# Kernel tuning notes

Measured on AMD Instinct MI355X. Metric: run time of the kernel, lower is better.

## Reference

```python
import jax, jax.numpy as jnp
import numpy as np

N_CELL, N_DRUG = 8192, 4096
E_CELL, E_DRUG = 262144, 131072
D_OUT = 128


def setup_inputs() -> dict:
    key = jax.random.key(0)
    ks = jax.random.split(key, 8)
    cell_feat = jax.random.normal(ks[0], (N_CELL, N_CELL), dtype=jnp.float32)
    drug_feat = jax.random.normal(ks[1], (N_DRUG, N_DRUG), dtype=jnp.float32)
    cell_edge = jax.random.randint(ks[2], (2, E_CELL), 0, N_CELL, dtype=jnp.int64)
    drug_edge = jax.random.randint(ks[3], (2, E_DRUG), 0, N_DRUG, dtype=jnp.int64)
    W_cell = jax.random.normal(ks[4], (N_CELL, D_OUT), dtype=jnp.float32) * 0.02
    W_drug = jax.random.normal(ks[5], (N_DRUG, D_OUT), dtype=jnp.float32) * 0.02
    b_cell = jnp.zeros((D_OUT,), dtype=jnp.float32)
    b_drug = jnp.zeros((D_OUT,), dtype=jnp.float32)
    return {"cell_feat": cell_feat, "cell_edge": cell_edge, "W_cell": W_cell,
            "b_cell": b_cell, "drug_feat": drug_feat, "drug_edge": drug_edge,
            "W_drug": W_drug, "b_drug": b_drug}


def _gcn_conv(x, edge, W, b):
    """PyG GCNConv with edge_weight = x[row, col] (as in GEncoder.forward),
    add_self_loops=True, symmetric normalization."""
    N = x.shape[0]
    row, col = edge[0], edge[1]
    ew = x[row, col]                                  # [E] gathered edge weights
    loop = jnp.arange(N)
    row = jnp.concatenate([row, loop])                # [E+N] self-loops appended
    col = jnp.concatenate([col, loop])
    ew = jnp.concatenate([ew, jnp.ones((N,), x.dtype)])
    deg = jax.ops.segment_sum(ew, col, num_segments=N)
    dinv = jnp.where(deg > 0, jax.lax.rsqrt(jnp.maximum(deg, 1e-30)), 0.0)
    norm = dinv[row] * ew * dinv[col]                 # [E+N]
    h = x @ W                                         # [N, D_OUT]
    msg = norm[:, None] * h[row]                      # gather + scale
    out = jax.ops.segment_sum(msg, col, num_segments=N) + b
    return jax.nn.relu(out)


def reference(cell_feat, cell_edge, W_cell, b_cell, drug_feat, drug_edge, W_drug, b_drug):
    cell_gcn = _gcn_conv(cell_feat, cell_edge, W_cell, b_cell)
    drug_gcn = _gcn_conv(drug_feat, drug_edge, W_drug, b_drug)
    return (cell_gcn, drug_gcn)
```

## Files before the change

kernel.cpp:

```cpp
#include <hip/hip_runtime.h>
#include <stdint.h>

#define N_CELL 8192
#define N_DRUG 4096
#define E_CELL 262144
#define E_DRUG 131072
#define DOUT   128

typedef float f32x4 __attribute__((ext_vector_type(4)));
typedef short s16x8 __attribute__((ext_vector_type(8)));

#define OFF_DEG_C   0u
#define OFF_DEG_D   8192u
#define OFF_CNT_C   12288u
#define OFF_CNT_D   20480u
#define OFF_CUR_C   24576u
#define OFF_CUR_D   32768u
#define OFF_START_C 36864u
#define OFF_START_D 45312u
#define OFF_EW_C    49664u
#define OFF_EW_D    311808u
#define OFF_SROW_C  442880u
#define OFF_SROW_D  705024u
#define OFF_SCOEF_C 836096u
#define OFF_SCOEF_D 1098240u
#define OFF_H_C     1229312u
#define OFF_H_D     2277888u
#define OFF_END     2802176u
#define WT_C_BYTE   (OFF_END * 4u)
#define WT_D_BYTE   (WT_C_BYTE + 128u * 8192u * 2u)
#define PART_C_BYTE 14354432u
#define PART_D_BYTE 31131648u
#define PART_END    35325952u

__device__ __forceinline__ unsigned short f2bf(float f) {
    union { float f; uint32_t u; } v; v.f = f;
    uint32_t u = v.u + 0x7fffu + ((v.u >> 16) & 1u);
    return (unsigned short)(u >> 16);
}

__device__ __forceinline__ s16x8 pack8(float4 x, float4 y) {
    union { float4 f; uint32_t u[4]; } a, b;
    a.f = x; b.f = y;
    union { uint32_t u[4]; s16x8 v; } r;
    r.u[0] = __builtin_amdgcn_perm(a.u[1] + 0x8000u, a.u[0] + 0x8000u, 0x07060302u);
    r.u[1] = __builtin_amdgcn_perm(a.u[3] + 0x8000u, a.u[2] + 0x8000u, 0x07060302u);
    r.u[2] = __builtin_amdgcn_perm(b.u[1] + 0x8000u, b.u[0] + 0x8000u, 0x07060302u);
    r.u[3] = __builtin_amdgcn_perm(b.u[3] + 0x8000u, b.u[2] + 0x8000u, 0x07060302u);
    return r.v;
}

__global__ __launch_bounds__(256) void k_prep(const float* __restrict__ Wc, const float* __restrict__ Wd,
                                              unsigned short* __restrict__ wtc, unsigned short* __restrict__ wtd,
                                              float* __restrict__ ws) {
    int bid = blockIdx.x, t = threadIdx.x;
    if (bid < 144) {
        int i = bid * 256 + t;
        ws[i] = (i < 12288) ? 1.0f : 0.0f;
        return;
    }
    if (bid < 1680) {
        size_t i = (size_t)(bid - 144) * 256 + t;
        ((float4*)(ws + OFF_H_C))[i] = make_float4(0.f, 0.f, 0.f, 0.f);
        return;
    }
    int tile = bid - 1680;
    const float* W; unsigned short* wt; int K;
    if (tile < 1024) { W = Wc; wt = wtc; K = N_CELL; }
    else             { W = Wd; wt = wtd; K = N_DRUG; tile -= 1024; }
    int tk = tile >> 2, tc = tile & 3;
    __shared__ float tl[32][33];
    int c = t & 31, r8 = t >> 5;
#pragma unroll
    for (int p = 0; p < 4; ++p) {
        int row = r8 + p * 8;
        tl[row][c] = W[(size_t)(tk * 32 + row) * DOUT + tc * 32 + c];
    }
    __syncthreads();
#pragma unroll
    for (int p = 0; p < 4; ++p) {
        int c2 = r8 + p * 8;
        wt[(size_t)(tc * 32 + c2) * K + tk * 32 + c] = f2bf(tl[c][c2]);
    }
}

__global__ __launch_bounds__(256) void k_edge(const float* __restrict__ xc, const int* __restrict__ ec,
                                              const float* __restrict__ xd, const int* __restrict__ ed,
                                              float* __restrict__ ws) {
    int i = blockIdx.x * 256 + threadIdx.x;
    const float* x; const int* edges; float* ew; float* deg; int* cnt; int N, E, idx;
    if (i < E_CELL) {
        idx = i; x = xc; edges = ec; N = N_CELL; E = E_CELL;
        ew = ws + OFF_EW_C; deg = ws + OFF_DEG_C; cnt = (int*)(ws + OFF_CNT_C);
    } else {
        idx = i - E_CELL; if (idx >= E_DRUG) return;
        x = xd; edges = ed; N = N_DRUG; E = E_DRUG;
        ew = ws + OFF_EW_D; deg = ws + OFF_DEG_D; cnt = (int*)(ws + OFF_CNT_D);
    }
    int r = edges[idx], c = edges[E + idx];
    float w = x[(size_t)r * N + c];
    ew[idx] = w;
    unsafeAtomicAdd(&deg[c], w);
    atomicAdd(&cnt[c], 1);
}

__global__ __launch_bounds__(256) void k_scan2(float* ws) {
    int bid = blockIdx.x, t = threadIdx.x;
    if (bid < 48) {
        int i = bid * 256 + t;
        float d = ws[i];
        ws[i] = d > 0.f ? rsqrtf(fmaxf(d, 1e-30f)) : 0.f;
        return;
    }
    const int* cnt; int* start; int N, chunk;
    if (bid == 48) { cnt = (const int*)(ws + OFF_CNT_C); start = (int*)(ws + OFF_START_C); N = N_CELL; chunk = 32; }
    else           { cnt = (const int*)(ws + OFF_CNT_D); start = (int*)(ws + OFF_START_D); N = N_DRUG; chunk = 16; }
    __shared__ int sums[256];
    int base = t * chunk;
    int s = 0;
    for (int j = 0; j < chunk; ++j) s += cnt[base + j];
    sums[t] = s; __syncthreads();
    for (int off = 1; off < 256; off <<= 1) {
        int v = (t >= off) ? sums[t - off] : 0;
        __syncthreads();
        sums[t] += v;
        __syncthreads();
    }
    int run = sums[t] - s;
    for (int j = 0; j < chunk; ++j) { start[base + j] = run; run += cnt[base + j]; }
    if (t == 255) start[N] = run;
}

__global__ __launch_bounds__(256) void k_fill(const int* __restrict__ ec, const int* __restrict__ ed,
                                              float* __restrict__ ws) {
    int i = blockIdx.x * 256 + threadIdx.x;
    const int* edges; const float* ew; const float* dinv; const int* start;
    int* cur; int* srow; float* scoef; int E, idx;
    if (i < E_CELL) {
        idx = i; edges = ec; E = E_CELL;
        ew = ws + OFF_EW_C; dinv = ws + OFF_DEG_C; start = (const int*)(ws + OFF_START_C);
        cur = (int*)(ws + OFF_CUR_C); srow = (int*)(ws + OFF_SROW_C); scoef = ws + OFF_SCOEF_C;
    } else {
        idx = i - E_CELL; if (idx >= E_DRUG) return;
        edges = ed; E = E_DRUG;
        ew = ws + OFF_EW_D; dinv = ws + OFF_DEG_D; start = (const int*)(ws + OFF_START_D);
        cur = (int*)(ws + OFF_CUR_D); srow = (int*)(ws + OFF_SROW_D); scoef = ws + OFF_SCOEF_D;
    }
    int r = edges[idx], c = edges[E + idx];
    float coef = dinv[r] * ew[idx] * dinv[c];
    int slot = start[c] + atomicAdd(&cur[c], 1);
    srow[slot] = r;
    scoef[slot] = coef;
}

__global__ __launch_bounds__(256, 6) void k_gemm(const float* __restrict__ xc, const float* __restrict__ xd,
                                                 const unsigned short* __restrict__ wtc,
                                                 const unsigned short* __restrict__ wtd,
                                                 float* __restrict__ ws,
                                                 float* __restrict__ partC, float* __restrict__ partD,
                                                 int usePart) {
    int bid = blockIdx.x, t = threadIdx.x;
    const float* x; const unsigned short* wt; float* hp; float* part; int K, mt, ch; size_t pstride;
    if (bid < 1024) {
        x = xc; wt = wtc; hp = ws + OFF_H_C; part = partC; K = N_CELL;
        mt = bid >> 2; ch = bid & 3; pstride = (size_t)N_CELL * DOUT;
    } else {
        int b = bid - 1024; x = xd; wt = wtd; hp = ws + OFF_H_D; part = partD; K = N_DRUG;
        mt = b >> 1; ch = b & 1; pstride = (size_t)N_DRUG * DOUT;
    }
    int k0 = ch * 2048;

    __shared__ alignas(16) unsigned short As[2][32][72];
    int lane = t & 63, wv = t >> 6;
    int l15 = lane & 15, l4 = lane >> 4;

    f32x4 acc[2][2] = {};

    int srow = t >> 3, sseg = t & 7;
    const float* abase = x + (size_t)(mt * 32 + srow) * K + k0 + sseg * 8;
    const unsigned short* bb = wt + (size_t)(wv * 32 + l15) * K + k0 + l4 * 8;
    const unsigned short* bb1 = bb + (size_t)16 * K;

    float4 X0, X1;

#define LOADA(KT) { const float4* _p = (const float4*)(abase + (size_t)(KT) * 64); \
                    X0 = _p[0]; X1 = _p[1]; }
#define WRITEA(BUF) { *(s16x8*)&As[BUF][srow][sseg * 8] = pack8(X0, X1); }

    LOADA(0);
    WRITEA(0);
    LOADA(1);
    __syncthreads();

#pragma unroll 1
    for (int kt = 0; kt < 32; ++kt) {
        s16x8 bq00 = *(const s16x8*)(bb  + (size_t)kt * 64);
        s16x8 bq01 = *(const s16x8*)(bb  + (size_t)kt * 64 + 32);
        s16x8 bq10 = *(const s16x8*)(bb1 + (size_t)kt * 64);
        s16x8 bq11 = *(const s16x8*)(bb1 + (size_t)kt * 64 + 32);
        if (kt < 31) {
            WRITEA((kt + 1) & 1);
            if (kt < 30) LOADA(kt + 2);
        }
        int bf = kt & 1;
        {
            s16x8 a0 = *(const s16x8*)&As[bf][l15][l4 * 8];
            s16x8 a1 = *(const s16x8*)&As[bf][16 + l15][l4 * 8];
            acc[0][0] = __builtin_amdgcn_mfma_f32_16x16x32_bf16(a0, bq00, acc[0][0], 0, 0, 0);
            acc[0][1] = __builtin_amdgcn_mfma_f32_16x16x32_bf16(a0, bq10, acc[0][1], 0, 0, 0);
            acc[1][0] = __builtin_amdgcn_mfma_f32_16x16x32_bf16(a1, bq00, acc[1][0], 0, 0, 0);
            acc[1][1] = __builtin_amdgcn_mfma_f32_16x16x32_bf16(a1, bq10, acc[1][1], 0, 0, 0);
        }
        {
            s16x8 a0 = *(const s16x8*)&As[bf][l15][32 + l4 * 8];
            s16x8 a1 = *(const s16x8*)&As[bf][16 + l15][32 + l4 * 8];
            acc[0][0] = __builtin_amdgcn_mfma_f32_16x16x32_bf16(a0, bq01, acc[0][0], 0, 0, 0);
            acc[0][1] = __builtin_amdgcn_mfma_f32_16x16x32_bf16(a0, bq11, acc[0][1], 0, 0, 0);
            acc[1][0] = __builtin_amdgcn_mfma_f32_16x16x32_bf16(a1, bq01, acc[1][0], 0, 0, 0);
            acc[1][1] = __builtin_amdgcn_mfma_f32_16x16x32_bf16(a1, bq11, acc[1][1], 0, 0, 0);
        }
        __syncthreads();
    }
#undef LOADA
#undef WRITEA
    if (usePart) {
        float* dst = part + (size_t)ch * pstride;
#pragma unroll
        for (int m = 0; m < 2; ++m)
#pragma unroll
            for (int n = 0; n < 2; ++n) {
                int col = wv * 32 + n * 16 + l15;
                int row = mt * 32 + m * 16 + l4 * 4;
#pragma unroll
                for (int j = 0; j < 4; ++j)
                    dst[(size_t)(row + j) * DOUT + col] = acc[m][n][j];
            }
    } else {
#pragma unroll
        for (int m = 0; m < 2; ++m)
#pragma unroll
            for (int n = 0; n < 2; ++n) {
                int col = wv * 32 + n * 16 + l15;
                int row = mt * 32 + m * 16 + l4 * 4;
#pragma unroll
                for (int j = 0; j < 4; ++j)
                    unsafeAtomicAdd(&hp[(size_t)(row + j) * DOUT + col], acc[m][n][j]);
            }
    }
}

__global__ __launch_bounds__(256) void k_reduce(const float* __restrict__ partC,
                                                const float* __restrict__ partD,
                                                float* __restrict__ ws) {
    int bid = blockIdx.x, t = threadIdx.x;
    if (bid < 1024) {
        size_t i = (size_t)bid * 256 + t;
        const f32x4* p = (const f32x4*)partC;
        f32x4 s = p[i] + p[i + 262144] + p[i + 2 * 262144] + p[i + 3 * 262144];
        ((f32x4*)(ws + OFF_H_C))[i] = s;
    } else {
        size_t i = (size_t)(bid - 1024) * 256 + t;
        const f32x4* p = (const f32x4*)partD;
        f32x4 s = p[i] + p[i + 131072];
        ((f32x4*)(ws + OFF_H_D))[i] = s;
    }
}

__global__ __launch_bounds__(256) void k_gather(const float* __restrict__ ws,
                                                const float* __restrict__ bc, const float* __restrict__ bd,
                                                float* __restrict__ out) {
    int wv = threadIdx.x >> 6, lane = threadIdx.x & 63;
    int g = blockIdx.x * 4 + wv;
    const float* h; const int* srow; const float* scoef; const int* start; const float* dinv;
    const float* bvec; float* outp; int node;
    if (g < N_CELL) {
        node = g; h = ws + OFF_H_C; srow = (const int*)(ws + OFF_SROW_C); scoef = ws + OFF_SCOEF_C;
        start = (const int*)(ws + OFF_START_C); dinv = ws + OFF_DEG_C; bvec = bc; outp = out;
    } else {
        node = g - N_CELL; if (node >= N_DRUG) return;
        h = ws + OFF_H_D; srow = (const int*)(ws + OFF_SROW_D); scoef = ws + OFF_SCOEF_D;
        start = (const int*)(ws + OFF_START_D); dinv = ws + OFF_DEG_D; bvec = bd;
        outp = out + (size_t)N_CELL * DOUT;
    }
    float di = dinv[node], sc = di * di;
    float2 v = ((const float2*)(h + (size_t)node * DOUT))[lane];
    float ax = sc * v.x, ay = sc * v.y;
    int s0 = start[node], s1 = start[node + 1];
    int e = s0;
    for (; e + 3 < s1; e += 4) {
        int r0 = srow[e];     float c0 = scoef[e];
        int r1 = srow[e + 1]; float c1 = scoef[e + 1];
        int r2 = srow[e + 2]; float c2 = scoef[e + 2];
        int r3 = srow[e + 3]; float c3 = scoef[e + 3];
        float2 u0 = ((const float2*)(h + (size_t)r0 * DOUT))[lane];
        float2 u1 = ((const float2*)(h + (size_t)r1 * DOUT))[lane];
        float2 u2 = ((const float2*)(h + (size_t)r2 * DOUT))[lane];
        float2 u3 = ((const float2*)(h + (size_t)r3 * DOUT))[lane];
        ax += c0 * u0.x + c1 * u1.x + c2 * u2.x + c3 * u3.x;
        ay += c0 * u0.y + c1 * u1.y + c2 * u2.y + c3 * u3.y;
    }
    for (; e < s1; ++e) {
        int r = srow[e]; float cf = scoef[e];
        float2 u = ((const float2*)(h + (size_t)r * DOUT))[lane];
        ax += cf * u.x; ay += cf * u.y;
    }
    float2 bb = ((const float2*)bvec)[lane];
    ax = fmaxf(ax + bb.x, 0.f);
    ay = fmaxf(ay + bb.y, 0.f);
    float2 o; o.x = ax; o.y = ay;
    ((float2*)outp)[(size_t)node * 64 + lane] = o;
}

extern "C" void kernel_launch(void* const* d_in, const int* in_sizes, int n_in,
                              void* d_out, int out_size, void* d_ws, size_t ws_size,
                              hipStream_t stream) {
    const float* cell_feat = (const float*)d_in[0];
    const int*   cell_edge = (const int*)d_in[1];
    const float* W_cell    = (const float*)d_in[2];
    const float* b_cell    = (const float*)d_in[3];
    const float* drug_feat = (const float*)d_in[4];
    const int*   drug_edge = (const int*)d_in[5];
    const float* W_drug    = (const float*)d_in[6];
    const float* b_drug    = (const float*)d_in[7];
    float* out = (float*)d_out;
    float* ws  = (float*)d_ws;
    unsigned short* wtc = (unsigned short*)((char*)d_ws + WT_C_BYTE);
    unsigned short* wtd = (unsigned short*)((char*)d_ws + WT_D_BYTE);
    float* partC = (float*)((char*)d_ws + PART_C_BYTE);
    float* partD = (float*)((char*)d_ws + PART_D_BYTE);
    int usePart = (ws_size >= (size_t)PART_END) ? 1 : 0;

    k_prep<<<3216, 256, 0, stream>>>(W_cell, W_drug, wtc, wtd, ws);
    k_edge<<<(E_CELL + E_DRUG) / 256, 256, 0, stream>>>(cell_feat, cell_edge, drug_feat, drug_edge, ws);
    k_scan2<<<50, 256, 0, stream>>>(ws);
    k_fill<<<1536, 256, 0, stream>>>(cell_edge, drug_edge, ws);
    k_gemm<<<1280, 256, 0, stream>>>(cell_feat, drug_feat, wtc, wtd, ws, partC, partD, usePart);
    if (usePart) k_reduce<<<1536, 256, 0, stream>>>(partC, partD, ws);
    k_gather<<<3072, 256, 0, stream>>>(ws, b_cell, b_drug, out);
}
```

Measured before the change: 240.6 us.

## Widen GEMM K-tile to 128 and double-buffer B fragments in registers

```diff
diff --git a/kernel.cpp b/kernel.cpp
--- a/kernel.cpp
+++ b/kernel.cpp
@@ -153,7 +153,7 @@
     scoef[slot] = coef;
 }
 
-__global__ __launch_bounds__(256, 6) void k_gemm(const float* __restrict__ xc, const float* __restrict__ xd,
+__global__ __launch_bounds__(256, 3) void k_gemm(const float* __restrict__ xc, const float* __restrict__ xd,
                                                  const unsigned short* __restrict__ wtc,
                                                  const unsigned short* __restrict__ wtd,
                                                  float* __restrict__ ws,
@@ -170,81 +170,110 @@
     }
     int k0 = ch * 2048;
 
-    __shared__ alignas(16) unsigned short As[2][32][72];
+    __shared__ alignas(16) unsigned short As[2][32][136];
     int lane = t & 63, wv = t >> 6;
     int l15 = lane & 15, l4 = lane >> 4;
 
-    f32x4 acc[2][2] = {};
+    f32x4 acc00 = {}, acc01 = {}, acc10 = {}, acc11 = {};
 
     int srow = t >> 3, sseg = t & 7;
-    const float* abase = x + (size_t)(mt * 32 + srow) * K + k0 + sseg * 8;
-    const unsigned short* bb = wt + (size_t)(wv * 32 + l15) * K + k0 + l4 * 8;
+    const float* abase = x + (size_t)(mt * 32 + srow) * K + k0 + sseg * 16;
+    const unsigned short* bb  = wt + (size_t)(wv * 32 + l15) * K + k0 + l4 * 8;
     const unsigned short* bb1 = bb + (size_t)16 * K;
 
-    float4 X0, X1;
-
-#define LOADA(KT) { const float4* _p = (const float4*)(abase + (size_t)(KT) * 64); \
-                    X0 = _p[0]; X1 = _p[1]; }
-#define WRITEA(BUF) { *(s16x8*)&As[BUF][srow][sseg * 8] = pack8(X0, X1); }
+    float4 X0, X1, X2, X3;
+    s16x8 BA0, BA1, BA2, BA3, BA4, BA5, BA6, BA7;
+    s16x8 BB0, BB1, BB2, BB3, BB4, BB5, BB6, BB7;
+
+#define LOADA(IT) { const float4* _p = (const float4*)(abase + (size_t)(IT) * 128); \
+                    X0 = _p[0]; X1 = _p[1]; X2 = _p[2]; X3 = _p[3]; }
+#define WRITEA(BUF) { *(s16x8*)&As[BUF][srow][sseg * 16]     = pack8(X0, X1); \
+                      *(s16x8*)&As[BUF][srow][sseg * 16 + 8] = pack8(X2, X3); }
+#define BLOADM(P0,P1,P2,P3,P4,P5,P6,P7, IT) { \
+    P0 = *(const s16x8*)(bb  + (size_t)(IT) * 128); \
+    P1 = *(const s16x8*)(bb  + (size_t)(IT) * 128 + 32); \
+    P2 = *(const s16x8*)(bb  + (size_t)(IT) * 128 + 64); \
+    P3 = *(const s16x8*)(bb  + (size_t)(IT) * 128 + 96); \
+    P4 = *(const s16x8*)(bb1 + (size_t)(IT) * 128); \
+    P5 = *(const s16x8*)(bb1 + (size_t)(IT) * 128 + 32); \
+    P6 = *(const s16x8*)(bb1 + (size_t)(IT) * 128 + 64); \
+    P7 = *(const s16x8*)(bb1 + (size_t)(IT) * 128 + 96); }
+#define COMPUTEM(BUF, B0,B1,B2,B3,B4,B5,B6,B7) { \
+    { s16x8 a0 = *(const s16x8*)&As[BUF][l15][l4 * 8]; \
+      s16x8 a1 = *(const s16x8*)&As[BUF][16 + l15][l4 * 8]; \
+      acc00 = __builtin_amdgcn_mfma_f32_16x16x32_bf16(a0, B0, acc00, 0, 0, 0); \
+      acc01 = __builtin_amdgcn_mfma_f32_16x16x32_bf16(a0, B4, acc01, 0, 0, 0); \
+      acc10 = __builtin_amdgcn_mfma_f32_16x16x32_bf16(a1, B0, acc10, 0, 0, 0); \
+      acc11 = __builtin_amdgcn_mfma_f32_16x16x32_bf16(a1, B4, acc11, 0, 0, 0); } \
+    { s16x8 a0 = *(const s16x8*)&As[BUF][l15][32 + l4 * 8]; \
+      s16x8 a1 = *(const s16x8*)&As[BUF][16 + l15][32 + l4 * 8]; \
+      acc00 = __builtin_amdgcn_mfma_f32_16x16x32_bf16(a0, B1, acc00, 0, 0, 0); \
+      acc01 = __builtin_amdgcn_mfma_f32_16x16x32_bf16(a0, B5, acc01, 0, 0, 0); \
+      acc10 = __builtin_amdgcn_mfma_f32_16x16x32_bf16(a1, B1, acc10, 0, 0, 0); \
+      acc11 = __builtin_amdgcn_mfma_f32_16x16x32_bf16(a1, B5, acc11, 0, 0, 0); } \
+    { s16x8 a0 = *(const s16x8*)&As[BUF][l15][64 + l4 * 8]; \
+      s16x8 a1 = *(const s16x8*)&As[BUF][16 + l15][64 + l4 * 8]; \
+      acc00 = __builtin_amdgcn_mfma_f32_16x16x32_bf16(a0, B2, acc00, 0, 0, 0); \
+      acc01 = __builtin_amdgcn_mfma_f32_16x16x32_bf16(a0, B6, acc01, 0, 0, 0); \
+      acc10 = __builtin_amdgcn_mfma_f32_16x16x32_bf16(a1, B2, acc10, 0, 0, 0); \
+      acc11 = __builtin_amdgcn_mfma_f32_16x16x32_bf16(a1, B6, acc11, 0, 0, 0); } \
+    { s16x8 a0 = *(const s16x8*)&As[BUF][l15][96 + l4 * 8]; \
+      s16x8 a1 = *(const s16x8*)&As[BUF][16 + l15][96 + l4 * 8]; \
+      acc00 = __builtin_amdgcn_mfma_f32_16x16x32_bf16(a0, B3, acc00, 0, 0, 0); \
+      acc01 = __builtin_amdgcn_mfma_f32_16x16x32_bf16(a0, B7, acc01, 0, 0, 0); \
+      acc10 = __builtin_amdgcn_mfma_f32_16x16x32_bf16(a1, B3, acc10, 0, 0, 0); \
+      acc11 = __builtin_amdgcn_mfma_f32_16x16x32_bf16(a1, B7, acc11, 0, 0, 0); } }
 
     LOADA(0);
     WRITEA(0);
     LOADA(1);
+    BLOADM(BA0,BA1,BA2,BA3,BA4,BA5,BA6,BA7, 0);
     __syncthreads();
 
 #pragma unroll 1
-    for (int kt = 0; kt < 32; ++kt) {
-        s16x8 bq00 = *(const s16x8*)(bb  + (size_t)kt * 64);
-        s16x8 bq01 = *(const s16x8*)(bb  + (size_t)kt * 64 + 32);
-        s16x8 bq10 = *(const s16x8*)(bb1 + (size_t)kt * 64);
-        s16x8 bq11 = *(const s16x8*)(bb1 + (size_t)kt * 64 + 32);
-        if (kt < 31) {
-            WRITEA((kt + 1) & 1);
-            if (kt < 30) LOADA(kt + 2);
+    for (int it2 = 0; it2 < 8; ++it2) {
+        int itE = it2 * 2, itO = itE + 1;
+        BLOADM(BB0,BB1,BB2,BB3,BB4,BB5,BB6,BB7, itO);
+        WRITEA(itO & 1);
+        if (itE < 14) LOADA(itE + 2);
+        COMPUTEM(itE & 1, BA0,BA1,BA2,BA3,BA4,BA5,BA6,BA7);
+        __syncthreads();
+        if (itO < 15) {
+            BLOADM(BA0,BA1,BA2,BA3,BA4,BA5,BA6,BA7, itO + 1);
+            WRITEA((itO + 1) & 1);
+            if (itO < 14) LOADA(itO + 2);
         }
-        int bf = kt & 1;
-        {
-            s16x8 a0 = *(const s16x8*)&As[bf][l15][l4 * 8];
-            s16x8 a1 = *(const s16x8*)&As[bf][16 + l15][l4 * 8];
-            acc[0][0] = __builtin_amdgcn_mfma_f32_16x16x32_bf16(a0, bq00, acc[0][0], 0, 0, 0);
-            acc[0][1] = __builtin_amdgcn_mfma_f32_16x16x32_bf16(a0, bq10, acc[0][1], 0, 0, 0);
-            acc[1][0] = __builtin_amdgcn_mfma_f32_16x16x32_bf16(a1, bq00, acc[1][0], 0, 0, 0);
-            acc[1][1] = __builtin_amdgcn_mfma_f32_16x16x32_bf16(a1, bq10, acc[1][1], 0, 0, 0);
-        }
-        {
-            s16x8 a0 = *(const s16x8*)&As[bf][l15][32 + l4 * 8];
-            s16x8 a1 = *(const s16x8*)&As[bf][16 + l15][32 + l4 * 8];
-            acc[0][0] = __builtin_amdgcn_mfma_f32_16x16x32_bf16(a0, bq01, acc[0][0], 0, 0, 0);
-            acc[0][1] = __builtin_amdgcn_mfma_f32_16x16x32_bf16(a0, bq11, acc[0][1], 0, 0, 0);
-            acc[1][0] = __builtin_amdgcn_mfma_f32_16x16x32_bf16(a1, bq01, acc[1][0], 0, 0, 0);
-            acc[1][1] = __builtin_amdgcn_mfma_f32_16x16x32_bf16(a1, bq11, acc[1][1], 0, 0, 0);
-        }
+        COMPUTEM(itO & 1, BB0,BB1,BB2,BB3,BB4,BB5,BB6,BB7);
         __syncthreads();
     }
 #undef LOADA
 #undef WRITEA
+#undef BLOADM
+#undef COMPUTEM
     if (usePart) {
         float* dst = part + (size_t)ch * pstride;
 #pragma unroll
         for (int m = 0; m < 2; ++m)
 #pragma unroll
             for (int n = 0; n < 2; ++n) {
+                f32x4 a = (m == 0) ? (n == 0 ? acc00 : acc01) : (n == 0 ? acc10 : acc11);
                 int col = wv * 32 + n * 16 + l15;
                 int row = mt * 32 + m * 16 + l4 * 4;
 #pragma unroll
                 for (int j = 0; j < 4; ++j)
-                    dst[(size_t)(row + j) * DOUT + col] = acc[m][n][j];
+                    dst[(size_t)(row + j) * DOUT + col] = a[j];
             }
     } else {
 #pragma unroll
         for (int m = 0; m < 2; ++m)
 #pragma unroll
             for (int n = 0; n < 2; ++n) {
+                f32x4 a = (m == 0) ? (n == 0 ? acc00 : acc01) : (n == 0 ? acc10 : acc11);
                 int col = wv * 32 + n * 16 + l15;
                 int row = mt * 32 + m * 16 + l4 * 4;
 #pragma unroll
                 for (int j = 0; j < 4; ++j)
-                    unsafeAtomicAdd(&hp[(size_t)(row + j) * DOUT + col], acc[m][n][j]);
+                    unsafeAtomicAdd(&hp[(size_t)(row + j) * DOUT + col], a[j]);
             }
     }
 }
```

Measured after the change: 228.2 us. 5.1% less time.

## Retile GEMM to 128-row blocks with LDS-staged weights and deeper split-K

Applied to the files above, without the earlier changes.

```diff
diff --git a/kernel.cpp b/kernel.cpp
--- a/kernel.cpp
+++ b/kernel.cpp
@@ -30,8 +30,8 @@
 #define WT_C_BYTE   (OFF_END * 4u)
 #define WT_D_BYTE   (WT_C_BYTE + 128u * 8192u * 2u)
 #define PART_C_BYTE 14354432u
-#define PART_D_BYTE 31131648u
-#define PART_END    35325952u
+#define PART_D_BYTE 47908864u
+#define PART_END    56297472u
 
 __device__ __forceinline__ unsigned short f2bf(float f) {
     union { float f; uint32_t u; } v; v.f = f;
@@ -153,98 +153,86 @@
     scoef[slot] = coef;
 }
 
-__global__ __launch_bounds__(256, 6) void k_gemm(const float* __restrict__ xc, const float* __restrict__ xd,
-                                                 const unsigned short* __restrict__ wtc,
-                                                 const unsigned short* __restrict__ wtd,
-                                                 float* __restrict__ ws,
-                                                 float* __restrict__ partC, float* __restrict__ partD,
-                                                 int usePart) {
+__global__ __launch_bounds__(256, 2) void k_gemm2(const float* __restrict__ xc, const float* __restrict__ xd,
+                                                  const unsigned short* __restrict__ wtc,
+                                                  const unsigned short* __restrict__ wtd,
+                                                  float* __restrict__ ws,
+                                                  float* __restrict__ partC, float* __restrict__ partD,
+                                                  int usePart) {
     int bid = blockIdx.x, t = threadIdx.x;
     const float* x; const unsigned short* wt; float* hp; float* part; int K, mt, ch; size_t pstride;
-    if (bid < 1024) {
+    if (bid < 512) {
         x = xc; wt = wtc; hp = ws + OFF_H_C; part = partC; K = N_CELL;
-        mt = bid >> 2; ch = bid & 3; pstride = (size_t)N_CELL * DOUT;
-    } else {
-        int b = bid - 1024; x = xd; wt = wtd; hp = ws + OFF_H_D; part = partD; K = N_DRUG;
-        mt = b >> 1; ch = b & 1; pstride = (size_t)N_DRUG * DOUT;
-    }
-    int k0 = ch * 2048;
-
-    __shared__ alignas(16) unsigned short As[2][32][72];
+        mt = bid >> 3; ch = bid & 7; pstride = (size_t)N_CELL * DOUT;
+    } else {
+        int b = bid - 512; x = xd; wt = wtd; hp = ws + OFF_H_D; part = partD; K = N_DRUG;
+        mt = b >> 2; ch = b & 3; pstride = (size_t)N_DRUG * DOUT;
+    }
+    int k0 = ch << 10;
+    int rowbase = mt * 128;
+
+    __shared__ unsigned short Bs[128 * 264];
     int lane = t & 63, wv = t >> 6;
     int l15 = lane & 15, l4 = lane >> 4;
 
-    f32x4 acc[2][2] = {};
-
-    int srow = t >> 3, sseg = t & 7;
-    const float* abase = x + (size_t)(mt * 32 + srow) * K + k0 + sseg * 8;
-    const unsigned short* bb = wt + (size_t)(wv * 32 + l15) * K + k0 + l4 * 8;
-    const unsigned short* bb1 = bb + (size_t)16 * K;
-
-    float4 X0, X1;
-
-#define LOADA(KT) { const float4* _p = (const float4*)(abase + (size_t)(KT) * 64); \
-                    X0 = _p[0]; X1 = _p[1]; }
-#define WRITEA(BUF) { *(s16x8*)&As[BUF][srow][sseg * 8] = pack8(X0, X1); }
-
-    LOADA(0);
-    WRITEA(0);
-    LOADA(1);
-    __syncthreads();
+    f32x4 acc[2][8] = {};
+    s16x8 af[2][8];
+
+    int bcol = t >> 1, bhalf = t & 1;
+    const unsigned short* bsrc = wt + (size_t)bcol * K + k0 + bhalf * 128;
+    unsigned bdst = (unsigned)bcol * 264u + (unsigned)bhalf * 128u;
+    int arow0 = rowbase + wv * 32 + l15;
+    const float* ap0 = x + (size_t)arow0 * K + k0 + l4 * 8;
+    const float* ap1 = ap0 + (size_t)16 * K;
 
 #pragma unroll 1
-    for (int kt = 0; kt < 32; ++kt) {
-        s16x8 bq00 = *(const s16x8*)(bb  + (size_t)kt * 64);
-        s16x8 bq01 = *(const s16x8*)(bb  + (size_t)kt * 64 + 32);
-        s16x8 bq10 = *(const s16x8*)(bb1 + (size_t)kt * 64);
-        s16x8 bq11 = *(const s16x8*)(bb1 + (size_t)kt * 64 + 32);
-        if (kt < 31) {
-            WRITEA((kt + 1) & 1);
-            if (kt < 30) LOADA(kt + 2);
+    for (int kc = 0; kc < 4; ++kc) {
+        __syncthreads();
+#pragma unroll
+        for (int j = 0; j < 16; ++j) {
+            s16x8 v = *(const s16x8*)(bsrc + kc * 256 + j * 8);
+            *(s16x8*)&Bs[bdst + (unsigned)j * 8u] = v;
         }
-        int bf = kt & 1;
-        {
-            s16x8 a0 = *(const s16x8*)&As[bf][l15][l4 * 8];
-            s16x8 a1 = *(const s16x8*)&As[bf][16 + l15][l4 * 8];
-            acc[0][0] = __builtin_amdgcn_mfma_f32_16x16x32_bf16(a0, bq00, acc[0][0], 0, 0, 0);
-            acc[0][1] = __builtin_amdgcn_mfma_f32_16x16x32_bf16(a0, bq10, acc[0][1], 0, 0, 0);
-            acc[1][0] = __builtin_amdgcn_mfma_f32_16x16x32_bf16(a1, bq00, acc[1][0], 0, 0, 0);
-            acc[1][1] = __builtin_amdgcn_mfma_f32_16x16x32_bf16(a1, bq10, acc[1][1], 0, 0, 0);
-        }
-        {
-            s16x8 a0 = *(const s16x8*)&As[bf][l15][32 + l4 * 8];
-            s16x8 a1 = *(const s16x8*)&As[bf][16 + l15][32 + l4 * 8];
-            acc[0][0] = __builtin_amdgcn_mfma_f32_16x16x32_bf16(a0, bq01, acc[0][0], 0, 0, 0);
-            acc[0][1] = __builtin_amdgcn_mfma_f32_16x16x32_bf16(a0, bq11, acc[0][1], 0, 0, 0);
-            acc[1][0] = __builtin_amdgcn_mfma_f32_16x16x32_bf16(a1, bq01, acc[1][0], 0, 0, 0);
-            acc[1][1] = __builtin_amdgcn_mfma_f32_16x16x32_bf16(a1, bq11, acc[1][1], 0, 0, 0);
+#pragma unroll
+        for (int js = 0; js < 8; ++js) {
+            const float4* p0 = (const float4*)(ap0 + kc * 256 + js * 32);
+            const float4* p1 = (const float4*)(ap1 + kc * 256 + js * 32);
+            af[0][js] = pack8(p0[0], p0[1]);
+            af[1][js] = pack8(p1[0], p1[1]);
         }
         __syncthreads();
-    }
-#undef LOADA
-#undef WRITEA
+#pragma unroll
+        for (int js = 0; js < 8; ++js) {
+#pragma unroll
+            for (int cg = 0; cg < 8; ++cg) {
+                s16x8 b = *(const s16x8*)&Bs[(unsigned)(cg * 16 + l15) * 264u + (unsigned)(js * 32 + l4 * 8)];
+                acc[0][cg] = __builtin_amdgcn_mfma_f32_16x16x32_bf16(af[0][js], b, acc[0][cg], 0, 0, 0);
+                acc[1][cg] = __builtin_amdgcn_mfma_f32_16x16x32_bf16(af[1][js], b, acc[1][cg], 0, 0, 0);
+            }
+        }
+    }
     if (usePart) {
         float* dst = part + (size_t)ch * pstride;
 #pragma unroll
         for (int m = 0; m < 2; ++m)
 #pragma unroll
-            for (int n = 0; n < 2; ++n) {
-                int col = wv * 32 + n * 16 + l15;
-                int row = mt * 32 + m * 16 + l4 * 4;
+            for (int cg = 0; cg < 8; ++cg) {
+                int col = cg * 16 + l15;
+                int row = rowbase + wv * 32 + m * 16 + l4 * 4;
 #pragma unroll
                 for (int j = 0; j < 4; ++j)
-                    dst[(size_t)(row + j) * DOUT + col] = acc[m][n][j];
+                    dst[(size_t)(row + j) * DOUT + col] = acc[m][cg][j];
             }
     } else {
 #pragma unroll
         for (int m = 0; m < 2; ++m)
 #pragma unroll
-            for (int n = 0; n < 2; ++n) {
-                int col = wv * 32 + n * 16 + l15;
-                int row = mt * 32 + m * 16 + l4 * 4;
+            for (int cg = 0; cg < 8; ++cg) {
+                int col = cg * 16 + l15;
+                int row = rowbase + wv * 32 + m * 16 + l4 * 4;
 #pragma unroll
                 for (int j = 0; j < 4; ++j)
-                    unsafeAtomicAdd(&hp[(size_t)(row + j) * DOUT + col], acc[m][n][j]);
+                    unsafeAtomicAdd(&hp[(size_t)(row + j) * DOUT + col], acc[m][cg][j]);
             }
     }
 }
@@ -256,12 +244,13 @@
     if (bid < 1024) {
         size_t i = (size_t)bid * 256 + t;
         const f32x4* p = (const f32x4*)partC;
-        f32x4 s = p[i] + p[i + 262144] + p[i + 2 * 262144] + p[i + 3 * 262144];
+        f32x4 s = p[i] + p[i + 262144] + p[i + 2 * 262144] + p[i + 3 * 262144]
+                + p[i + 4 * 262144] + p[i + 5 * 262144] + p[i + 6 * 262144] + p[i + 7 * 262144];
         ((f32x4*)(ws + OFF_H_C))[i] = s;
     } else {
         size_t i = (size_t)(bid - 1024) * 256 + t;
         const f32x4* p = (const f32x4*)partD;
-        f32x4 s = p[i] + p[i + 131072];
+        f32x4 s = p[i] + p[i + 131072] + p[i + 2 * 131072] + p[i + 3 * 131072];
         ((f32x4*)(ws + OFF_H_D))[i] = s;
     }
 }
@@ -334,7 +323,7 @@
     k_edge<<<(E_CELL + E_DRUG) / 256, 256, 0, stream>>>(cell_feat, cell_edge, drug_feat, drug_edge, ws);
     k_scan2<<<50, 256, 0, stream>>>(ws);
     k_fill<<<1536, 256, 0, stream>>>(cell_edge, drug_edge, ws);
-    k_gemm<<<1280, 256, 0, stream>>>(cell_feat, drug_feat, wtc, wtd, ws, partC, partD, usePart);
+    k_gemm2<<<640, 256, 0, stream>>>(cell_feat, drug_feat, wtc, wtd, ws, partC, partD, usePart);
     if (usePart) k_reduce<<<1536, 256, 0, stream>>>(partC, partD, ws);
     k_gather<<<3072, 256, 0, stream>>>(ws, b_cell, b_drug, out);
 }
```

New measurement: 288.5 us. 1.2x slower.
